# Kernel tuning notes

Hardware: AMD Instinct MI355X
Metric: run time of the kernel (lower is better)

## Reference

```python
import jax, jax.numpy as jnp
import numpy as np

B, S, DIN = 16, 960, 7
HID, HEADS, LAYERS = 512, 8, 4
PERIODS = (24, 48, 96)
OUT_LEN = 96
HEAD_DIM = HID // HEADS
FFN = 4 * HID


def setup_inputs() -> dict:
    key = jax.random.key(0)
    ks = jax.random.split(key, 20)
    sc = 0.02
    return {
        "x": jax.random.normal(ks[0], (B, S, DIN), dtype=jnp.float32),
        "input_proj_w": jax.random.normal(ks[1], (HID, DIN), dtype=jnp.float32) * sc,
        "input_proj_b": jnp.zeros((HID,), dtype=jnp.float32),
        "in_proj_w": jax.random.normal(ks[2], (LAYERS, 3 * HID, HID), dtype=jnp.float32) * sc,
        "in_proj_b": jnp.zeros((LAYERS, 3 * HID), dtype=jnp.float32),
        "out_proj_w": jax.random.normal(ks[3], (LAYERS, HID, HID), dtype=jnp.float32) * sc,
        "out_proj_b": jnp.zeros((LAYERS, HID), dtype=jnp.float32),
        "ffn_w1": jax.random.normal(ks[4], (LAYERS, FFN, HID), dtype=jnp.float32) * sc,
        "ffn_b1": jnp.zeros((LAYERS, FFN), dtype=jnp.float32),
        "ffn_w2": jax.random.normal(ks[5], (LAYERS, HID, FFN), dtype=jnp.float32) * sc,
        "ffn_b2": jnp.zeros((LAYERS, HID), dtype=jnp.float32),
        "ln1_w": jnp.ones((LAYERS, HID), dtype=jnp.float32),
        "ln1_b": jnp.zeros((LAYERS, HID), dtype=jnp.float32),
        "ln2_w": jnp.ones((LAYERS, HID), dtype=jnp.float32),
        "ln2_b": jnp.zeros((LAYERS, HID), dtype=jnp.float32),
        "output_proj_w": jax.random.normal(ks[6], (1, HID), dtype=jnp.float32) * sc,
        "output_proj_b": jnp.zeros((1,), dtype=jnp.float32),
    }


def _layer_norm(x, w, b, eps=1e-5):
    mu = jnp.mean(x, axis=-1, keepdims=True)
    var = jnp.mean(jnp.square(x - mu), axis=-1, keepdims=True)
    return (x - mu) * jax.lax.rsqrt(var + eps) * w + b


def _mha(x, wqkv, bqkv, wo, bo):
    # x: [N, P, H]; self-attention, PyTorch nn.MultiheadAttention math (eval mode)
    N, P, _ = x.shape
    qkv = x @ wqkv.T + bqkv                      # [N, P, 3H]
    q, k, v = jnp.split(qkv, 3, axis=-1)
    q = q.reshape(N, P, HEADS, HEAD_DIM)
    k = k.reshape(N, P, HEADS, HEAD_DIM)
    v = v.reshape(N, P, HEADS, HEAD_DIM)
    scores = jnp.einsum("nqhd,nkhd->nhqk", q, k) / jnp.sqrt(jnp.float32(HEAD_DIM))
    attn = jax.nn.softmax(scores, axis=-1)
    out = jnp.einsum("nhqk,nkhd->nqhd", attn, v).reshape(N, P, HID)
    return out @ wo.T + bo


def _times_block(x, period, wqkv, bqkv, wo, bo, w1, b1, w2, b2, g1, be1, g2, be2):
    # x: [B, S, H], S % period == 0. Batch all period slices together
    # (replaces the original Python loop over num_periods).
    Bc, Sc, H = x.shape
    xb = x.reshape(Bc * (Sc // period), period, H)
    attn = _mha(xb, wqkv, bqkv, wo, bo)
    xb = _layer_norm(xb + attn, g1, be1)
    ffn = jax.nn.gelu(xb @ w1.T + b1, approximate=False) @ w2.T + b2
    xb = _layer_norm(xb + ffn, g2, be2)
    return xb.reshape(Bc, Sc, H)


def reference(x, input_proj_w, input_proj_b, in_proj_w, in_proj_b, out_proj_w,
              out_proj_b, ffn_w1, ffn_b1, ffn_w2, ffn_b2, ln1_w, ln1_b,
              ln2_w, ln2_b, output_proj_w, output_proj_b):
    h = x @ input_proj_w.T + input_proj_b        # [B, S, H]
    branches = []
    for period in PERIODS:
        ph = h
        for l in range(LAYERS):
            ph = _times_block(ph, period,
                              in_proj_w[l], in_proj_b[l], out_proj_w[l], out_proj_b[l],
                              ffn_w1[l], ffn_b1[l], ffn_w2[l], ffn_b2[l],
                              ln1_w[l], ln1_b[l], ln2_w[l], ln2_b[l])
        branches.append(ph)
    h = jnp.mean(jnp.stack(branches, axis=0), axis=0)     # [B, S, H]
    out = h @ output_proj_w.T + output_proj_b             # [B, S, 1]
    # AdaptiveAvgPool1d(OUT_LEN) with S % OUT_LEN == 0 -> uniform block mean
    out = out.reshape(B, OUT_LEN, S // OUT_LEN, 1).mean(axis=2)  # [B, OUT_LEN, 1]
    return out
```

## Files before the change

### kernel.cpp

```cpp
#include <hip/hip_runtime.h>
#include <hip/hip_bf16.h>

typedef __bf16 bf16;
typedef __attribute__((ext_vector_type(8))) __bf16 bf16x8;
typedef __attribute__((ext_vector_type(4))) __bf16 bf16x4;
typedef __attribute__((ext_vector_type(4))) float f32x4;

#define TOKENS 15360
#define HID    512
#define FFN_D  2048
#define QKV_D  1536

__device__ __forceinline__ float gelu_erf(float x) {
  const float z = fabsf(x) * 0.70710678118654752f;
#if __has_builtin(__builtin_amdgcn_rcpf)
  const float t = __builtin_amdgcn_rcpf(fmaf(0.3275911f, z, 1.f));
#else
  const float t = 1.f / fmaf(0.3275911f, z, 1.f);
#endif
  float p = fmaf(1.061405429f, t, -1.453152027f);
  p = fmaf(p, t, 1.421413741f);
  p = fmaf(p, t, -0.284496736f);
  p = fmaf(p, t, 0.254829592f);
  p *= t;
  const float e  = __expf(-z * z);
  const float er = fmaf(-p, e, 1.f);
  return 0.5f * x * (1.f + copysignf(er, x));
}

__global__ __launch_bounds__(256) void cvt_kernel(const float* __restrict__ src,
                                                  bf16* __restrict__ dst, int n4) {
  const int i = (blockIdx.x * 256 + threadIdx.x);
  if (i >= n4) return;
  const float4 v = ((const float4*)src)[i];
  bf16x4 d = {(bf16)v.x, (bf16)v.y, (bf16)v.z, (bf16)v.w};
  *(bf16x4*)(dst + (size_t)i * 4) = d;
}

__global__ __launch_bounds__(256) void cvt_w2_kernel(const float* __restrict__ src,
                                                     bf16* __restrict__ dst, int n4) {
  const int i = (blockIdx.x * 256 + threadIdx.x);
  if (i >= n4) return;
  const int f  = i * 4;
  const int ln = f >> 11;
  const int c2 = f & 2047;
  const int h  = c2 >> 10;
  const int c  = c2 & 1023;
  const int l  = ln >> 9;
  const int n  = ln & 511;
  const float4 v = ((const float4*)src)[i];
  bf16x4 d = {(bf16)v.x, (bf16)v.y, (bf16)v.z, (bf16)v.w};
  *(bf16x4*)(dst + ((((size_t)(l * 2 + h) * 512 + n) << 10) + c)) = d;
}

#define EPI_BIAS_BF16     0
#define EPI_BIAS_RES_BF16 1
#define EPI_BIAS_GELU     2
#define EPI_RES_BF16      3

template <int EPI>
__global__ __launch_bounds__(256) void gemm_bt(
    const bf16* __restrict__ A, const bf16* __restrict__ W,
    const float* __restrict__ bias, const bf16* __restrict__ R,
    bf16* __restrict__ out, int M, int N, int K) {
  __shared__ __align__(16) bf16 As[2 * 128 * 32];
  __shared__ __align__(16) bf16 Bs[2 * 128 * 32];

  const int tid  = threadIdx.x;
  const int lane = tid & 63;
  const int wv   = tid >> 6;
  const int li   = lane & 15;
  const int qd   = lane >> 4;
  const int mw   = (wv & 1) << 6;
  const int nw   = (wv >> 1) << 6;

  const int NB  = gridDim.x;
  const int nwg = NB * gridDim.y;
  int lid = blockIdx.y * NB + blockIdx.x;
  if ((nwg & 7) == 0) lid = (lid & 7) * (nwg >> 3) + (lid >> 3);
  const int n0 = (lid % NB) << 7;
  const int m0 = (lid / NB) << 7;

  f32x4 acc[4][4];
#pragma unroll
  for (int i = 0; i < 4; ++i)
#pragma unroll
    for (int j = 0; j < 4; ++j) acc[i][j] = (f32x4){0.f, 0.f, 0.f, 0.f};

  const bf16* pa[2];
  const bf16* pb[2];
  int off[2];
#pragma unroll
  for (int it = 0; it < 2; ++it) {
    const int q    = it * 256 + tid;
    const int r    = q >> 2;
    const int c    = q & 3;
    const int koff = (c ^ ((r >> 1) & 3)) << 3;
    pa[it]  = A + (size_t)(m0 + r) * K + koff;
    pb[it]  = W + (size_t)(n0 + r) * K + koff;
    off[it] = (it * 256 + (tid & 192)) * 8;
  }

  auto stage = [&](int buf) {
#pragma unroll
    for (int it = 0; it < 2; ++it) {
      __builtin_amdgcn_global_load_lds(
          (const __attribute__((address_space(1))) unsigned int*)pa[it],
          (__attribute__((address_space(3))) unsigned int*)(As + buf * 4096 + off[it]),
          16, 0, 0);
      pa[it] += 32;
    }
#pragma unroll
    for (int it = 0; it < 2; ++it) {
      __builtin_amdgcn_global_load_lds(
          (const __attribute__((address_space(1))) unsigned int*)pb[it],
          (__attribute__((address_space(3))) unsigned int*)(Bs + buf * 4096 + off[it]),
          16, 0, 0);
      pb[it] += 32;
    }
  };

  auto compute = [&](int buf) {
    const bf16* Ab = As + buf * 4096;
    const bf16* Bb = Bs + buf * 4096;
    const int sl = (qd ^ ((li >> 1) & 3)) << 3;
    bf16x8 af[4], bfv[4];
#pragma unroll
    for (int i = 0; i < 4; ++i)
      af[i] = *(const bf16x8*)(Ab + (mw + i * 16 + li) * 32 + sl);
#pragma unroll
    for (int j = 0; j < 4; ++j)
      bfv[j] = *(const bf16x8*)(Bb + (nw + j * 16 + li) * 32 + sl);
#pragma unroll
    for (int i = 0; i < 4; ++i)
#pragma unroll
      for (int j = 0; j < 4; ++j)
        acc[i][j] = __builtin_amdgcn_mfma_f32_16x16x32_bf16(af[i], bfv[j],
                                                            acc[i][j], 0, 0, 0);
  };

  stage(0);
  int cur = 0;
  for (int k0 = 0; k0 < K - 32; k0 += 32) {
    stage(cur ^ 1);
    asm volatile("s_waitcnt vmcnt(4)" ::: "memory");
    __builtin_amdgcn_s_barrier();
    asm volatile("" ::: "memory");
    compute(cur);
    asm volatile("" ::: "memory");
    __builtin_amdgcn_s_barrier();
    asm volatile("" ::: "memory");
    cur ^= 1;
  }
  asm volatile("s_waitcnt vmcnt(0)" ::: "memory");
  __builtin_amdgcn_s_barrier();
  asm volatile("" ::: "memory");
  compute(cur);

#pragma unroll
  for (int i = 0; i < 4; ++i) {
    const int mrow = m0 + mw + i * 16 + qd * 4;
#pragma unroll
    for (int j = 0; j < 4; ++j) {
      const int ncol = n0 + nw + j * 16 + li;
      float bv = 0.f;
      if (EPI != EPI_RES_BF16) bv = bias[ncol];
#pragma unroll
      for (int r = 0; r < 4; ++r) {
        const size_t off2 = (size_t)(mrow + r) * N + ncol;
        float v = acc[i][j][r] + bv;
        if (EPI == EPI_BIAS_RES_BF16 || EPI == EPI_RES_BF16) v += (float)R[off2];
        out[off2] = (EPI == EPI_BIAS_GELU) ? (bf16)gelu_erf(v) : (bf16)v;
      }
    }
  }
}

template <int P>
__global__ __launch_bounds__(256) void attn_kernel(const bf16* __restrict__ qkv,
                                                   bf16* __restrict__ out) {
  constexpr int PP   = ((P + 15) / 16) * 16;
  constexpr int PK   = ((PP + 31) / 32) * 32;
  constexpr int MT   = PP / 16;
  constexpr int SSTR = PP + 2;
  constexpr int VSTR = PK + 8;
  constexpr int PSTR = PK + 8;
  constexpr int G    = (P * 8 <= 256) ? 8 : ((P * 4 <= 256) ? 4 : 2);

  __shared__ __align__(16) bf16 QK[2 * PP * 64];
  __shared__ __align__(16) bf16 Vt[64 * VSTR];
  __shared__ __align__(16) float Sm[PP * SSTR];
  __shared__ float rsum[PP];

  bf16* Qs = QK;
  bf16* Ks = QK + PP * 64;
  bf16* Ps = QK;

  const int tid  = threadIdx.x;
  const int lane = tid & 63;
  const int wv   = tid >> 6;
  const int li   = lane & 15;
  const int qd   = lane >> 4;
  const int n    = blockIdx.x >> 3;
  const int h    = blockIdx.x & 7;
  const bf16* base = qkv + (size_t)n * P * QKV_D + h * 64;

  for (int t = tid; t < P * 8; t += 256) {
    const int r = t >> 3, c = t & 7;
    const bf16x8 qv = *(const bf16x8*)(base + (size_t)r * QKV_D + c * 8);
    const bf16x8 kv = *(const bf16x8*)(base + (size_t)r * QKV_D + 512 + c * 8);
    *(bf16x8*)(Qs + r * 64 + ((c ^ (r & 7)) * 8)) = qv;
    *(bf16x8*)(Ks + r * 64 + ((c ^ (r & 7)) * 8)) = kv;
  }
  for (int t = tid; t < P * 8; t += 256) {
    const int j = t % P, dc = t / P;
    const bf16x8 vv = *(const bf16x8*)(base + (size_t)j * QKV_D + 1024 + dc * 8);
#pragma unroll
    for (int u = 0; u < 8; ++u) Vt[(dc * 8 + u) * VSTR + j] = vv[u];
  }
  if constexpr (PK > P) {
    for (int t = tid; t < 64 * (PK - P); t += 256) {
      const int d = t / (PK - P), j = P + t % (PK - P);
      Vt[d * VSTR + j] = (bf16)0.f;
    }
  }
  __syncthreads();

  for (int t = wv; t < MT * MT; t += 4) {
    const int ti = t / MT, tj = t % MT;
    f32x4 acc = (f32x4){0.f, 0.f, 0.f, 0.f};
#pragma unroll
    for (int ks = 0; ks < 2; ++ks) {
      const int ck = ks * 4 + qd;
      const int ar = ti * 16 + li;
      const int br = tj * 16 + li;
      const bf16x8 af = *(const bf16x8*)(Qs + ar * 64 + ((ck ^ (ar & 7)) * 8));
      const bf16x8 bv = *(const bf16x8*)(Ks + br * 64 + ((ck ^ (br & 7)) * 8));
      acc = __builtin_amdgcn_mfma_f32_16x16x32_bf16(af, bv, acc, 0, 0, 0);
    }
#pragma unroll
    for (int r = 0; r < 4; ++r)
      Sm[(ti * 16 + qd * 4 + r) * SSTR + tj * 16 + li] = acc[r];
  }
  __syncthreads();

  if (tid < P * G) {
    const int row = tid / G, g = tid % G;
    const float* srow = Sm + row * SSTR;
    bf16* prow = Ps + row * PSTR;
    float mx = -1e30f;
    for (int j = g; j < P; j += G) mx = fmaxf(mx, srow[j]);
#pragma unroll
    for (int m = G >> 1; m; m >>= 1) mx = fmaxf(mx, __shfl_xor(mx, m, 64));
    mx *= 0.125f;
    float sum = 0.f;
    for (int j = g; j < P; j += G) {
      const float e = __expf(srow[j] * 0.125f - mx);
      sum += e;
      prow[j] = (bf16)e;
    }
#pragma unroll
    for (int m = G >> 1; m; m >>= 1) sum += __shfl_xor(sum, m, 64);
    for (int j = P + g; j < PK; j += G) prow[j] = (bf16)0.f;
    if (g == 0) rsum[row] = 1.f / sum;
  }
  __syncthreads();

  for (int t = wv; t < MT * 4; t += 4) {
    const int ti = t >> 2, td = t & 3;
    f32x4 acc = (f32x4){0.f, 0.f, 0.f, 0.f};
#pragma unroll
    for (int ks = 0; ks < PK / 32; ++ks) {
      const int ck = ks * 4 + qd;
      const bf16x8 af = *(const bf16x8*)(Ps + (ti * 16 + li) * PSTR + ck * 8);
      const bf16x8 bv = *(const bf16x8*)(Vt + (td * 16 + li) * VSTR + ck * 8);
      acc = __builtin_amdgcn_mfma_f32_16x16x32_bf16(af, bv, acc, 0, 0, 0);
    }
#pragma unroll
    for (int r = 0; r < 4; ++r) {
      const int row = ti * 16 + qd * 4 + r;
      if (row < P)
        out[(size_t)(n * P + row) * HID + h * 64 + td * 16 + li] =
            (bf16)(acc[r] * rsum[row]);
    }
  }
}

__global__ __launch_bounds__(256) void ln_kernel(const bf16* __restrict__ Y,
                                                 const float* __restrict__ w,
                                                 const float* __restrict__ b,
                                                 bf16* __restrict__ X) {
  const int row  = blockIdx.x * 4 + (threadIdx.x >> 6);
  const int lane = threadIdx.x & 63;
  const bf16x8 yv = *(const bf16x8*)(Y + (size_t)row * HID + 8 * lane);
  float y[8];
#pragma unroll
  for (int u = 0; u < 8; ++u) y[u] = (float)yv[u];
  float s = 0.f, s2 = 0.f;
#pragma unroll
  for (int u = 0; u < 8; ++u) { s += y[u]; s2 += y[u] * y[u]; }
#pragma unroll
  for (int off = 32; off > 0; off >>= 1) {
    s  += __shfl_xor(s, off, 64);
    s2 += __shfl_xor(s2, off, 64);
  }
  const float mean = s * (1.f / 512.f);
  const float var  = s2 * (1.f / 512.f) - mean * mean;
  const float rstd = rsqrtf(var + 1e-5f);
  const float4 w0 = ((const float4*)w)[2 * lane];
  const float4 w1 = ((const float4*)w)[2 * lane + 1];
  const float4 b0 = ((const float4*)b)[2 * lane];
  const float4 b1 = ((const float4*)b)[2 * lane + 1];
  const float wr[8] = {w0.x, w0.y, w0.z, w0.w, w1.x, w1.y, w1.z, w1.w};
  const float br[8] = {b0.x, b0.y, b0.z, b0.w, b1.x, b1.y, b1.z, b1.w};
  bf16x8 o;
#pragma unroll
  for (int u = 0; u < 8; ++u) o[u] = (bf16)((y[u] - mean) * rstd * wr[u] + br[u]);
  *(bf16x8*)(X + (size_t)row * HID + 8 * lane) = o;
}

__global__ __launch_bounds__(256) void inproj_kernel(const float* __restrict__ x,
                                                     const float* __restrict__ w,
                                                     const float* __restrict__ b,
                                                     bf16* __restrict__ h,
                                                     int nbr) {
  const int idx = blockIdx.x * 256 + threadIdx.x;
  const int r = idx >> 9, o = idx & 511;
  float s = b[o];
#pragma unroll
  for (int k = 0; k < 7; ++k) s += x[r * 7 + k] * w[o * 7 + k];
  const bf16 bv = (bf16)s;
  for (int q = 0; q < nbr; ++q) h[idx + (size_t)q * TOKENS * HID] = bv;
}

__global__ __launch_bounds__(256) void outdot_kernel(const bf16* __restrict__ X,
                                                     const float* __restrict__ w,
                                                     float* __restrict__ acc,
                                                     int first) {
  const int row  = blockIdx.x * 4 + (threadIdx.x >> 6);
  const int lane = threadIdx.x & 63;
  const bf16* xr = X + (size_t)row * HID;
  const bf16x8 xa = *(const bf16x8*)(xr + 8 * lane);
  const float4 wa = ((const float4*)w)[2 * lane];
  const float4 wb = ((const float4*)w)[2 * lane + 1];
  float s = (float)xa[0] * wa.x + (float)xa[1] * wa.y + (float)xa[2] * wa.z +
            (float)xa[3] * wa.w + (float)xa[4] * wb.x + (float)xa[5] * wb.y +
            (float)xa[6] * wb.z + (float)xa[7] * wb.w;
#pragma unroll
  for (int off = 32; off > 0; off >>= 1) s += __shfl_xor(s, off, 64);
  if (lane == 0) acc[row] = first ? s : (acc[row] + s);
}

__global__ __launch_bounds__(256) void pool_kernel(const float* __restrict__ acc,
                                                   const float* __restrict__ ob,
                                                   float* __restrict__ out) {
  const int idx = blockIdx.x * 256 + threadIdx.x;
  if (idx >= 16 * 96) return;
  const int bb = idx / 96, o = idx % 96;
  float s = 0.f;
#pragma unroll
  for (int j = 0; j < 10; ++j) s += acc[bb * 960 + o * 10 + j];
  out[idx] = s * (1.f / 30.f) + ob[0];
}

extern "C" void kernel_launch(void* const* d_in, const int* in_sizes, int n_in,
                              void* d_out, int out_size, void* d_ws,
                              size_t ws_size, hipStream_t stream) {
  const float* x          = (const float*)d_in[0];
  const float* ip_w       = (const float*)d_in[1];
  const float* ip_b       = (const float*)d_in[2];
  const float* in_proj_w  = (const float*)d_in[3];
  const float* in_proj_b  = (const float*)d_in[4];
  const float* out_proj_w = (const float*)d_in[5];
  const float* out_proj_b = (const float*)d_in[6];
  const float* ffn_w1     = (const float*)d_in[7];
  const float* ffn_b1     = (const float*)d_in[8];
  const float* ffn_w2     = (const float*)d_in[9];
  const float* ffn_b2     = (const float*)d_in[10];
  const float* ln1_w      = (const float*)d_in[11];
  const float* ln1_b      = (const float*)d_in[12];
  const float* ln2_w      = (const float*)d_in[13];
  const float* ln2_b      = (const float*)d_in[14];
  const float* op_w       = (const float*)d_in[15];
  const float* op_b       = (const float*)d_in[16];

  char* p = (char*)d_ws;
  bf16* Wq = (bf16*)p; p += (size_t)4 * QKV_D * HID * 2;
  bf16* Wo = (bf16*)p; p += (size_t)4 * HID * HID * 2;
  bf16* W1 = (bf16*)p; p += (size_t)4 * FFN_D * HID * 2;
  bf16* W2 = (bf16*)p; p += (size_t)4 * HID * FFN_D * 2;
  float* ACC = (float*)p; p += (size_t)TOKENS * 4;
  const size_t remain = ws_size - (size_t)(p - (char*)d_ws);

  const size_t T3 = 3 * (size_t)TOKENS;
  const size_t need_unsplit = T3 * HID * 2 + T3 * (size_t)FFN_D * 2 + T3 * HID * 2;
  const size_t need_split   = T3 * HID * 2 + T3 * (size_t)FFN_D * 2;
  const size_t need_seq     = (size_t)TOKENS * HID * 2 + (size_t)TOKENS * FFN_D * 2;
  const bool unsplit = remain >= need_unsplit;
  const bool batched = remain >= need_split;
  if (!batched && remain < need_seq) return;

  {
    const int nq = 4 * QKV_D * HID / 4, no = 4 * HID * HID / 4,
              n1 = 4 * FFN_D * HID / 4, n2 = 4 * HID * FFN_D / 4;
    cvt_kernel<<<(nq + 255) / 256, 256, 0, stream>>>(in_proj_w, Wq, nq);
    cvt_kernel<<<(no + 255) / 256, 256, 0, stream>>>(out_proj_w, Wo, no);
    cvt_kernel<<<(n1 + 255) / 256, 256, 0, stream>>>(ffn_w1, W1, n1);
    if (unsplit)
      cvt_kernel<<<(n2 + 255) / 256, 256, 0, stream>>>(ffn_w2, W2, n2);
    else
      cvt_w2_kernel<<<(n2 + 255) / 256, 256, 0, stream>>>(ffn_w2, W2, n2);
  }

  static const int periods[3] = {24, 48, 96};
  auto launch_attn = [&](int P, const bf16* q, bf16* o) {
    const int nblk = (TOKENS / P) * 8;
    if (P == 24)      attn_kernel<24><<<nblk, 256, 0, stream>>>(q, o);
    else if (P == 48) attn_kernel<48><<<nblk, 256, 0, stream>>>(q, o);
    else              attn_kernel<96><<<nblk, 256, 0, stream>>>(q, o);
  };

  auto run_layer = [&](int l, int M, int qkvM, bf16* X, bf16* QKV, bf16* ATT,
                       bf16* YB, bf16* H, bool all_br, int br, bool unspl) {
    const int MB = M / 128;
    gemm_bt<EPI_BIAS_BF16><<<dim3(QKV_D / 128, qkvM / 128), 256, 0, stream>>>(
        X, Wq + (size_t)l * QKV_D * HID, in_proj_b + l * QKV_D, nullptr,
        QKV, qkvM, QKV_D, HID);
    if (all_br) {
      for (int b2 = 0; b2 < 3; ++b2) {
        const bf16* q = QKV + (qkvM == M ? (size_t)b2 * TOKENS * QKV_D : 0);
        launch_attn(periods[b2], q, ATT + (size_t)b2 * TOKENS * HID);
      }
    } else {
      launch_attn(periods[br], QKV, ATT);
    }
    gemm_bt<EPI_BIAS_RES_BF16><<<dim3(HID / 128, MB), 256, 0, stream>>>(
        ATT, Wo + (size_t)l * HID * HID, out_proj_b + l * HID, X, YB,
        M, HID, HID);
    ln_kernel<<<M / 4, 256, 0, stream>>>(YB, ln1_w + l * HID, ln1_b + l * HID, X);
    if (unspl) {
      gemm_bt<EPI_BIAS_GELU><<<dim3(FFN_D / 128, MB), 256, 0, stream>>>(
          X, W1 + (size_t)l * FFN_D * HID, ffn_b1 + l * FFN_D, nullptr,
          H, M, FFN_D, HID);
      gemm_bt<EPI_BIAS_RES_BF16><<<dim3(HID / 128, MB), 256, 0, stream>>>(
          H, W2 + (size_t)l * HID * FFN_D, ffn_b2 + l * HID, X, YB,
          M, HID, FFN_D);
    } else {
      gemm_bt<EPI_BIAS_GELU><<<dim3(1024 / 128, MB), 256, 0, stream>>>(
          X, W1 + (size_t)l * FFN_D * HID, ffn_b1 + l * FFN_D, nullptr,
          H, M, 1024, HID);
      gemm_bt<EPI_BIAS_RES_BF16><<<dim3(HID / 128, MB), 256, 0, stream>>>(
          H, W2 + (size_t)(l * 2 + 0) * HID * 1024, ffn_b2 + l * HID, X, YB,
          M, HID, 1024);
      gemm_bt<EPI_BIAS_GELU><<<dim3(1024 / 128, MB), 256, 0, stream>>>(
          X, W1 + (size_t)l * FFN_D * HID + (size_t)1024 * HID,
          ffn_b1 + l * FFN_D + 1024, nullptr, H, M, 1024, HID);
      gemm_bt<EPI_RES_BF16><<<dim3(HID / 128, MB), 256, 0, stream>>>(
          H, W2 + (size_t)(l * 2 + 1) * HID * 1024, nullptr, YB, YB,
          M, HID, 1024);
    }
    ln_kernel<<<M / 4, 256, 0, stream>>>(YB, ln2_w + l * HID, ln2_b + l * HID, X);
  };

  if (batched) {
    bf16* X   = (bf16*)p; p += T3 * HID * 2;
    bf16* BUF = (bf16*)p; p += T3 * (size_t)FFN_D * 2;
    bf16* QKV = BUF;
    bf16* ATT = BUF + T3 * QKV_D;
    bf16* H, * YB;
    if (unsplit) {
      H  = BUF;
      YB = (bf16*)p;
    } else {
      H  = BUF;
      YB = BUF + T3 * 1024;
    }
    const int M = (int)T3;

    inproj_kernel<<<TOKENS * HID / 256, 256, 0, stream>>>(x, ip_w, ip_b, X, 3);
    for (int l = 0; l < 4; ++l)
      run_layer(l, M, l == 0 ? TOKENS : M, X, QKV, ATT, YB, H, true, 0, unsplit);
    for (int br = 0; br < 3; ++br)
      outdot_kernel<<<TOKENS / 4, 256, 0, stream>>>(
          X + (size_t)br * TOKENS * HID, op_w, ACC, br == 0);
  } else {
    bf16* X   = (bf16*)p; p += (size_t)TOKENS * HID * 2;
    bf16* SCR = (bf16*)p; p += (size_t)TOKENS * FFN_D * 2;
    bf16* QKV = SCR;
    bf16* ATT = SCR + (size_t)TOKENS * QKV_D;
    bf16* H   = SCR;
    bf16* YB  = SCR + (size_t)TOKENS * 1024;
    const int M = TOKENS;

    for (int br = 0; br < 3; ++br) {
      inproj_kernel<<<TOKENS * HID / 256, 256, 0, stream>>>(x, ip_w, ip_b, X, 1);
      for (int l = 0; l < 4; ++l)
        run_layer(l, M, M, X, QKV, ATT, YB, H, false, br, false);
      outdot_kernel<<<TOKENS / 4, 256, 0, stream>>>(X, op_w, ACC, br == 0);
    }
  }
  pool_kernel<<<6, 256, 0, stream>>>(ACC, op_b, (float*)d_out);
}
```

Before: 2.247 ms.

## Rewrite GEMM as 256x256 tile, 8-wave kernel with quadrant-pipelined staging

The bf16 GEMM moves from 128x128 tiles with 4 waves and BK=32 to 256x256 tiles with 8 waves and BK=64. Loads are staged in half-tiles interleaved with MFMA quadrants, using s_setprio around the MFMA blocks and an XOR swizzle across 8 chunks. The aim is more data reuse per byte loaded and better overlap of global-to-LDS copies with compute. In exchange it uses 128KB of LDS per block and launches fewer workgroups, which can cause tail and occupancy problems on small grids such as the N=512 GEMMs.

```diff
diff --git a/kernel.cpp b/kernel.cpp
--- a/kernel.cpp
+++ b/kernel.cpp
@@ -59,110 +59,166 @@
 #define EPI_RES_BF16      3
 
 template <int EPI>
-__global__ __launch_bounds__(256) void gemm_bt(
+__global__ __launch_bounds__(512, 2) void gemm_bt(
     const bf16* __restrict__ A, const bf16* __restrict__ W,
     const float* __restrict__ bias, const bf16* __restrict__ R,
     bf16* __restrict__ out, int M, int N, int K) {
-  __shared__ __align__(16) bf16 As[2 * 128 * 32];
-  __shared__ __align__(16) bf16 Bs[2 * 128 * 32];
+  __shared__ __align__(16) bf16 As[2 * 2 * 128 * 64];
+  __shared__ __align__(16) bf16 Bs[2 * 2 * 128 * 64];
 
   const int tid  = threadIdx.x;
   const int lane = tid & 63;
   const int wv   = tid >> 6;
   const int li   = lane & 15;
   const int qd   = lane >> 4;
-  const int mw   = (wv & 1) << 6;
-  const int nw   = (wv >> 1) << 6;
+  const int wm   = wv >> 2;
+  const int wn   = wv & 3;
 
   const int NB  = gridDim.x;
   const int nwg = NB * gridDim.y;
   int lid = blockIdx.y * NB + blockIdx.x;
   if ((nwg & 7) == 0) lid = (lid & 7) * (nwg >> 3) + (lid >> 3);
-  const int n0 = (lid % NB) << 7;
-  const int m0 = (lid / NB) << 7;
-
-  f32x4 acc[4][4];
-#pragma unroll
-  for (int i = 0; i < 4; ++i)
+  const int n0 = (lid % NB) << 8;
+  const int m0 = (lid / NB) << 8;
+
+  f32x4 acc[8][4];
+#pragma unroll
+  for (int i = 0; i < 8; ++i)
 #pragma unroll
     for (int j = 0; j < 4; ++j) acc[i][j] = (f32x4){0.f, 0.f, 0.f, 0.f};
 
-  const bf16* pa[2];
-  const bf16* pb[2];
-  int off[2];
+  int garow[2], gbrow[2], ko[2], wu[2];
 #pragma unroll
   for (int it = 0; it < 2; ++it) {
-    const int q    = it * 256 + tid;
-    const int r    = q >> 2;
-    const int c    = q & 3;
-    const int koff = (c ^ ((r >> 1) & 3)) << 3;
-    pa[it]  = A + (size_t)(m0 + r) * K + koff;
-    pb[it]  = W + (size_t)(n0 + r) * K + koff;
-    off[it] = (it * 256 + (tid & 192)) * 8;
-  }
-
-  auto stage = [&](int buf) {
-#pragma unroll
-    for (int it = 0; it < 2; ++it) {
+    const int q  = it * 512 + tid;
+    const int rp = q >> 3;
+    const int c  = q & 7;
+    garow[it] = (rp >> 6) * 128 + (rp & 63);
+    gbrow[it] = (rp >> 5) * 64 + (rp & 31);
+    ko[it]    = (c ^ (rp & 7)) << 3;
+    wu[it]    = (it * 512 + (tid & 448)) * 8;
+  }
+
+  auto stageA = [&](int buf, int ih, int k0) {
+#pragma unroll
+    for (int it = 0; it < 2; ++it)
       __builtin_amdgcn_global_load_lds(
-          (const __attribute__((address_space(1))) unsigned int*)pa[it],
-          (__attribute__((address_space(3))) unsigned int*)(As + buf * 4096 + off[it]),
+          (const __attribute__((address_space(1))) unsigned int*)(
+              A + (size_t)(m0 + garow[it] + ih * 64) * K + k0 + ko[it]),
+          (__attribute__((address_space(3))) unsigned int*)(
+              As + (buf * 2 + ih) * 8192 + wu[it]),
           16, 0, 0);
-      pa[it] += 32;
-    }
-#pragma unroll
-    for (int it = 0; it < 2; ++it) {
+  };
+  auto stageB = [&](int buf, int jh, int k0) {
+#pragma unroll
+    for (int it = 0; it < 2; ++it)
       __builtin_amdgcn_global_load_lds(
-          (const __attribute__((address_space(1))) unsigned int*)pb[it],
-          (__attribute__((address_space(3))) unsigned int*)(Bs + buf * 4096 + off[it]),
+          (const __attribute__((address_space(1))) unsigned int*)(
+              W + (size_t)(n0 + gbrow[it] + jh * 32) * K + k0 + ko[it]),
+          (__attribute__((address_space(3))) unsigned int*)(
+              Bs + (buf * 2 + jh) * 8192 + wu[it]),
           16, 0, 0);
-      pb[it] += 32;
-    }
-  };
-
-  auto compute = [&](int buf) {
-    const bf16* Ab = As + buf * 4096;
-    const bf16* Bb = Bs + buf * 4096;
-    const int sl = (qd ^ ((li >> 1) & 3)) << 3;
-    bf16x8 af[4], bfv[4];
+  };
+
+  bf16x8 af[4][2], bfv[2][2];
+
+  auto dsA = [&](int buf, int ih) {
+    const bf16* base = As + (buf * 2 + ih) * 8192 + (wm * 64) * 64;
 #pragma unroll
     for (int i = 0; i < 4; ++i)
-      af[i] = *(const bf16x8*)(Ab + (mw + i * 16 + li) * 32 + sl);
-#pragma unroll
-    for (int j = 0; j < 4; ++j)
-      bfv[j] = *(const bf16x8*)(Bb + (nw + j * 16 + li) * 32 + sl);
-#pragma unroll
-    for (int i = 0; i < 4; ++i)
-#pragma unroll
-      for (int j = 0; j < 4; ++j)
-        acc[i][j] = __builtin_amdgcn_mfma_f32_16x16x32_bf16(af[i], bfv[j],
-                                                            acc[i][j], 0, 0, 0);
-  };
-
-  stage(0);
-  int cur = 0;
-  for (int k0 = 0; k0 < K - 32; k0 += 32) {
-    stage(cur ^ 1);
-    asm volatile("s_waitcnt vmcnt(4)" ::: "memory");
-    __builtin_amdgcn_s_barrier();
-    asm volatile("" ::: "memory");
-    compute(cur);
-    asm volatile("" ::: "memory");
-    __builtin_amdgcn_s_barrier();
-    asm volatile("" ::: "memory");
-    cur ^= 1;
-  }
-  asm volatile("s_waitcnt vmcnt(0)" ::: "memory");
+#pragma unroll
+      for (int ks = 0; ks < 2; ++ks) {
+        const int ck = ks * 4 + qd;
+        af[i][ks] = *(const bf16x8*)(base + (i * 16 + li) * 64 +
+                                     ((ck ^ (li & 7)) << 3));
+      }
+  };
+  auto dsB = [&](int buf, int jh) {
+    const bf16* base = Bs + (buf * 2 + jh) * 8192 + (wn * 32) * 64;
+#pragma unroll
+    for (int j = 0; j < 2; ++j)
+#pragma unroll
+      for (int ks = 0; ks < 2; ++ks) {
+        const int ck = ks * 4 + qd;
+        bfv[j][ks] = *(const bf16x8*)(base + (j * 16 + li) * 64 +
+                                      ((ck ^ (li & 7)) << 3));
+      }
+  };
+  auto mfma16 = [&](int ih, int jh) {
+    __builtin_amdgcn_s_setprio(1);
+#pragma unroll
+    for (int ks = 0; ks < 2; ++ks)
+#pragma unroll
+      for (int i = 0; i < 4; ++i)
+#pragma unroll
+        for (int j = 0; j < 2; ++j)
+          acc[ih * 4 + i][jh * 2 + j] = __builtin_amdgcn_mfma_f32_16x16x32_bf16(
+              af[i][ks], bfv[j][ks], acc[ih * 4 + i][jh * 2 + j], 0, 0, 0);
+    __builtin_amdgcn_s_setprio(0);
+  };
+
+  const int nt = K >> 6;
+  stageA(0, 0, 0); stageB(0, 0, 0); stageB(0, 1, 0); stageA(0, 1, 0);
+  stageA(1, 0, 64); stageB(1, 1, 64);
+  asm volatile("s_waitcnt vmcnt(4)" ::: "memory");
   __builtin_amdgcn_s_barrier();
   asm volatile("" ::: "memory");
-  compute(cur);
-
-#pragma unroll
-  for (int i = 0; i < 4; ++i) {
-    const int mrow = m0 + mw + i * 16 + qd * 4;
+
+  for (int t = 0; t < nt; ++t) {
+    const int b  = t & 1;
+    const int nb = b ^ 1;
+    const int k1 = (t + 1) << 6;
+    const int k2 = (t + 2) << 6;
+    const bool s1 = (t + 1 < nt);
+    const bool s2 = (t + 2 < nt);
+
+    dsA(b, 0); dsB(b, 0);
+    if (s1) stageA(nb, 1, k1);
+    asm volatile("" ::: "memory");
+    __builtin_amdgcn_s_barrier();
+    mfma16(0, 0);
+    asm volatile("" ::: "memory");
+    __builtin_amdgcn_s_barrier();
+    asm volatile("" ::: "memory");
+
+    dsB(b, 1);
+    if (s1) stageB(nb, 0, k1);
+    asm volatile("" ::: "memory");
+    __builtin_amdgcn_s_barrier();
+    mfma16(0, 1);
+    asm volatile("" ::: "memory");
+    __builtin_amdgcn_s_barrier();
+    asm volatile("" ::: "memory");
+
+    dsA(b, 1);
+    if (s2) stageA(b, 0, k2);
+    asm volatile("" ::: "memory");
+    __builtin_amdgcn_s_barrier();
+    mfma16(1, 1);
+    asm volatile("" ::: "memory");
+    __builtin_amdgcn_s_barrier();
+    asm volatile("" ::: "memory");
+
+    dsB(b, 0);
+    if (s2) stageB(b, 1, k2);
+    asm volatile("" ::: "memory");
+    __builtin_amdgcn_s_barrier();
+    mfma16(1, 0);
+    if (s1) {
+      if (s2) asm volatile("s_waitcnt vmcnt(4)" ::: "memory");
+      else    asm volatile("s_waitcnt vmcnt(0)" ::: "memory");
+    }
+    asm volatile("" ::: "memory");
+    __builtin_amdgcn_s_barrier();
+    asm volatile("" ::: "memory");
+  }
+
+#pragma unroll
+  for (int i = 0; i < 8; ++i) {
+    const int mrow = m0 + wm * 128 + i * 16 + qd * 4;
 #pragma unroll
     for (int j = 0; j < 4; ++j) {
-      const int ncol = n0 + nw + j * 16 + li;
+      const int ncol = n0 + wn * 64 + j * 16 + li;
       float bv = 0.f;
       if (EPI != EPI_RES_BF16) bv = bias[ncol];
 #pragma unroll
@@ -422,8 +478,8 @@
 
   auto run_layer = [&](int l, int M, int qkvM, bf16* X, bf16* QKV, bf16* ATT,
                        bf16* YB, bf16* H, bool all_br, int br, bool unspl) {
-    const int MB = M / 128;
-    gemm_bt<EPI_BIAS_BF16><<<dim3(QKV_D / 128, qkvM / 128), 256, 0, stream>>>(
+    const int MB = M / 256;
+    gemm_bt<EPI_BIAS_BF16><<<dim3(QKV_D / 256, qkvM / 256), 512, 0, stream>>>(
         X, Wq + (size_t)l * QKV_D * HID, in_proj_b + l * QKV_D, nullptr,
         QKV, qkvM, QKV_D, HID);
     if (all_br) {
@@ -434,28 +490,28 @@
     } else {
       launch_attn(periods[br], QKV, ATT);
     }
-    gemm_bt<EPI_BIAS_RES_BF16><<<dim3(HID / 128, MB), 256, 0, stream>>>(
+    gemm_bt<EPI_BIAS_RES_BF16><<<dim3(HID / 256, MB), 512, 0, stream>>>(
         ATT, Wo + (size_t)l * HID * HID, out_proj_b + l * HID, X, YB,
         M, HID, HID);
     ln_kernel<<<M / 4, 256, 0, stream>>>(YB, ln1_w + l * HID, ln1_b + l * HID, X);
     if (unspl) {
-      gemm_bt<EPI_BIAS_GELU><<<dim3(FFN_D / 128, MB), 256, 0, stream>>>(
+      gemm_bt<EPI_BIAS_GELU><<<dim3(FFN_D / 256, MB), 512, 0, stream>>>(
           X, W1 + (size_t)l * FFN_D * HID, ffn_b1 + l * FFN_D, nullptr,
           H, M, FFN_D, HID);
-      gemm_bt<EPI_BIAS_RES_BF16><<<dim3(HID / 128, MB), 256, 0, stream>>>(
+      gemm_bt<EPI_BIAS_RES_BF16><<<dim3(HID / 256, MB), 512, 0, stream>>>(
           H, W2 + (size_t)l * HID * FFN_D, ffn_b2 + l * HID, X, YB,
           M, HID, FFN_D);
     } else {
-      gemm_bt<EPI_BIAS_GELU><<<dim3(1024 / 128, MB), 256, 0, stream>>>(
+      gemm_bt<EPI_BIAS_GELU><<<dim3(1024 / 256, MB), 512, 0, stream>>>(
           X, W1 + (size_t)l * FFN_D * HID, ffn_b1 + l * FFN_D, nullptr,
           H, M, 1024, HID);
-      gemm_bt<EPI_BIAS_RES_BF16><<<dim3(HID / 128, MB), 256, 0, stream>>>(
+      gemm_bt<EPI_BIAS_RES_BF16><<<dim3(HID / 256, MB), 512, 0, stream>>>(
           H, W2 + (size_t)(l * 2 + 0) * HID * 1024, ffn_b2 + l * HID, X, YB,
           M, HID, 1024);
-      gemm_bt<EPI_BIAS_GELU><<<dim3(1024 / 128, MB), 256, 0, stream>>>(
+      gemm_bt<EPI_BIAS_GELU><<<dim3(1024 / 256, MB), 512, 0, stream>>>(
           X, W1 + (size_t)l * FFN_D * HID + (size_t)1024 * HID,
           ffn_b1 + l * FFN_D + 1024, nullptr, H, M, 1024, HID);
-      gemm_bt<EPI_RES_BF16><<<dim3(HID / 128, MB), 256, 0, stream>>>(
+      gemm_bt<EPI_RES_BF16><<<dim3(HID / 256, MB), 512, 0, stream>>>(
           H, W2 + (size_t)(l * 2 + 1) * HID * 1024, nullptr, YB, YB,
           M, HID, 1024);
     }
```

Measured after the change: 2.272 ms. No clear change (+1.1%).
